# Performance work log

Hardware: AMD Instinct MI355X
Metric: run time of the kernel (lower is better)

The kernel has to match this reference:

```python
import jax, jax.numpy as jnp
import numpy as np

SEGMENTS = 64
SU2NDIM = 16
N = 16  # SU(2^4) matrix dimension
BATCH = 128


def setup_inputs() -> dict:
    key = jax.random.key(0)
    # Small scale keeps expm well-conditioned (skew-ish generators in practice)
    x = 0.1 * jax.random.normal(key, (BATCH, SEGMENTS * SU2NDIM, N, N), dtype=jnp.float32)
    return {"x": x}


def _batched_expm(a):
    # a: [..., N, N] -> expm over last two dims
    flat = a.reshape((-1, N, N))
    ex = jax.vmap(jax.scipy.linalg.expm)(flat)
    return ex.reshape(a.shape)


def reference(x):
    # maintensor = expm(-x), reversed along axis 0 (faithful to source)
    m = _batched_expm(-x)            # [B, S*D, N, N]
    m = m[::-1]                      # tf.reverse(maintensor, [0])
    b = m.shape[0]
    # tf.split along axis 1 into SEGMENTS contiguous chunks of SU2NDIM
    m = m.reshape(b, SEGMENTS, SU2NDIM, N, N)
    # Sequential chain product per segment: U = M[D-1] @ ... @ M[1] @ M[0] @ I
    ms = jnp.moveaxis(m, 2, 0)       # [D, B, S, N, N]
    u0 = jnp.broadcast_to(jnp.eye(N, dtype=x.dtype), (b, SEGMENTS, N, N))
    def step(u, mj):
        return mj @ u, None
    u, _ = jax.lax.scan(step, u0, ms)
    return u                         # [B, SEGMENTS, N, N] == transpose([1,0,2,3]) of stacked list
```

## Files before the change

### kernel.cpp

```cpp
#include <hip/hip_runtime.h>

typedef float f32x4 __attribute__((ext_vector_type(4)));
typedef short s16x8 __attribute__((ext_vector_type(8)));
typedef unsigned int uint;
typedef uint u32x4 __attribute__((ext_vector_type(4)));

union Frag {
  u32x4 u;
  s16x8 s;
};

__device__ __forceinline__ uint packhi(float f0, float f1) {
  uint a = __float_as_uint(f0) + 0x8000u;
  uint b = __float_as_uint(f1) + 0x8000u;
  return __builtin_amdgcn_perm(b, a, 0x07060302u);
}

__device__ __forceinline__ void split2(float f0, float f1, uint& hi, uint& lo) {
  uint a0 = __float_as_uint(f0) + 0x8000u;
  uint a1 = __float_as_uint(f1) + 0x8000u;
  hi = __builtin_amdgcn_perm(a1, a0, 0x07060302u);
  float h0 = __uint_as_float(a0 & 0xFFFF0000u);
  float h1 = __uint_as_float(a1 & 0xFFFF0000u);
  lo = packhi(f0 - h0, f1 - h1);
}

#define CFENCE() __asm__ __volatile__("" ::: "memory")

__device__ __forceinline__ f32x4 expm_negT(const float* __restrict__ A,
                                           uint* __restrict__ hb, int lo,
                                           int g, int gt, bool low, f32x4 idm) {
  float c0 = A[(8 * gt + 0) * 16 + lo], c1 = A[(8 * gt + 1) * 16 + lo];
  float c2 = A[(8 * gt + 2) * 16 + lo], c3 = A[(8 * gt + 3) * 16 + lo];
  float c4 = A[(8 * gt + 4) * 16 + lo], c5 = A[(8 * gt + 5) * 16 + lo];
  float c6 = A[(8 * gt + 6) * 16 + lo], c7 = A[(8 * gt + 7) * 16 + lo];
  f32x4 xr = *(const f32x4*)(A + lo * 16 + 4 * g);
  uint h, lw;
  Frag xa;
  split2(c0, c1, h, lw); xa.u[0] = low ? h : lw;
  split2(c2, c3, h, lw); xa.u[1] = low ? h : lw;
  split2(c4, c5, h, lw); xa.u[2] = low ? h : lw;
  split2(c6, c7, h, lw); xa.u[3] = low ? h : lw;
  f32x4 t;
#pragma unroll
  for (int i = 0; i < 4; ++i)
    t[i] = fmaf(1.f / 720.f, xr[i], (-1.f / 120.f) * idm[i]);
  const float SK[5] = {1.f / 24.f, -1.f / 6.f, 0.5f, -1.f, 1.f};
  uint* wp = hb + lo * 12 + 2 * g;
  const uint* rp = hb + lo * 12 + 4 * gt;
#pragma unroll
  for (int k = 0; k < 5; ++k) {
    wp[0] = packhi(t[0], t[1]);
    wp[1] = packhi(t[2], t[3]);
    CFENCE();
    Frag tb;
    tb.u = *(const u32x4*)rp;
    CFENCE();
    f32x4 acc = idm * SK[k];
    t = __builtin_amdgcn_mfma_f32_16x16x32_bf16(xa.s, tb.s, acc, 0, 0, 0);
  }
  return t;
}

__global__ __launch_bounds__(256, 8) void unitary_kernel(
    const float* __restrict__ x, float* __restrict__ out) {
  __shared__ uint HB[4][192];
  __shared__ uint PE[4][320];
  __shared__ uint PU[4][320];

  const int tid = threadIdx.x;
  const int w = tid >> 6;
  const int l = tid & 63;
  const int lo = l & 15;
  const int g = l >> 4;
  const int gt = g & 1;
  const bool low = g < 2;

  uint* hb = HB[w];
  uint* pe = PE[w];
  uint* pu = PU[w];

  const int ch = blockIdx.x * 4 + w;
  const float* xb =
      x + ((size_t)(127 - (ch >> 6)) * 1024 + (size_t)(ch & 63) * 16) * 256;

  f32x4 idm;
  idm[0] = (4 * g + 0 == lo) ? 1.f : 0.f;
  idm[1] = (4 * g + 1 == lo) ? 1.f : 0.f;
  idm[2] = (4 * g + 2 == lo) ? 1.f : 0.f;
  idm[3] = (4 * g + 3 == lo) ? 1.f : 0.f;

  Frag ifr;
  {
    uint v = ((lo >> 3) == gt) ? (0x3F80u << (16 * (lo & 1))) : 0u;
    int slot = (lo >> 1) & 3;
    ifr.u[0] = (slot == 0) ? v : 0u;
    ifr.u[1] = (slot == 1) ? v : 0u;
    ifr.u[2] = (slot == 2) ? v : 0u;
    ifr.u[3] = (slot == 3) ? v : 0u;
  }

  uint* pew = pe + lo * 20 + 4 * g;
  const uint* pea = pe + lo * 20 + 8 * gt + (low ? 0 : 2);
  uint* puw = pu + lo * 20 + 4 * g;
  const uint* pub = pu + lo * 20 + 8 * gt;

  f32x4 uc;
#pragma unroll 1
  for (int j = 0; j < 16; ++j) {
    f32x4 et = expm_negT(xb + j * 256, hb, lo, g, gt, low, idm);
    uint h0, l0, h1, l1;
    split2(et[0], et[1], h0, l0);
    split2(et[2], et[3], h1, l1);
    *(u32x4*)pew = (u32x4){h0, h1, l0, l1};
    if (j) {
      split2(uc[0], uc[1], h0, l0);
      split2(uc[2], uc[3], h1, l1);
      *(u32x4*)puw = (u32x4){h0, h1, l0, l1};
    }
    CFENCE();
    Frag ea;
    ea.u[0] = pea[0];
    ea.u[1] = pea[1];
    ea.u[2] = pea[4];
    ea.u[3] = pea[5];
    f32x4 z = {0.f, 0.f, 0.f, 0.f};
    if (j) {
      Frag b1, b2;
      b1.u[0] = pub[0];
      b1.u[1] = pub[1];
      b1.u[2] = pub[4];
      b1.u[3] = pub[5];
      b2.u[0] = pub[2];
      b2.u[1] = pub[3];
      b2.u[2] = pub[6];
      b2.u[3] = pub[7];
      CFENCE();
      f32x4 t1 = __builtin_amdgcn_mfma_f32_16x16x32_bf16(ea.s, b1.s, z, 0, 0, 0);
      uc = __builtin_amdgcn_mfma_f32_16x16x32_bf16(ea.s, b2.s, t1, 0, 0, 0);
    } else {
      CFENCE();
      uc = __builtin_amdgcn_mfma_f32_16x16x32_bf16(ea.s, ifr.s, z, 0, 0, 0);
    }
  }

  float* op = out + (size_t)ch * 256;
  op[(4 * g + 0) * 16 + lo] = uc[0];
  op[(4 * g + 1) * 16 + lo] = uc[1];
  op[(4 * g + 2) * 16 + lo] = uc[2];
  op[(4 * g + 3) * 16 + lo] = uc[3];
}

extern "C" void kernel_launch(void* const* d_in, const int* in_sizes, int n_in,
                              void* d_out, int out_size, void* d_ws,
                              size_t ws_size, hipStream_t stream) {
  const float* x = (const float*)d_in[0];
  float* out = (float*)d_out;
  unitary_kernel<<<dim3(2048), dim3(256), 0, stream>>>(x, out);
}
```

Measured before the change: 190.9 us.

## Replace LDS fragment transposes with permlane16/32 swap register shuffles

Fragment redistribution between MFMA output and input layouts was staged through per-wave shared memory (write, fence, read). It now uses v_permlane32_swap and v_permlane16_swap cross-lane exchanges held entirely in registers, for the Taylor-series operand, the exp matrix and the running product. This removes LDS traffic and its latency from the serial dependency chain, at the cost of several permlane instructions per exchange. It also frees all shared memory, which may help occupancy.

```diff
diff --git a/kernel.cpp b/kernel.cpp
--- a/kernel.cpp
+++ b/kernel.cpp
@@ -4,6 +4,7 @@
 typedef short s16x8 __attribute__((ext_vector_type(8)));
 typedef unsigned int uint;
 typedef uint u32x4 __attribute__((ext_vector_type(4)));
+typedef uint u32x2 __attribute__((ext_vector_type(2)));
 
 union Frag {
   u32x4 u;
@@ -25,10 +26,46 @@
   lo = packhi(f0 - h0, f1 - h1);
 }
 
-#define CFENCE() __asm__ __volatile__("" ::: "memory")
+__device__ __forceinline__ u32x2 swap32(uint a, uint b) {
+#if __has_builtin(__builtin_amdgcn_permlane32_swap)
+  return __builtin_amdgcn_permlane32_swap(a, b, false, false);
+#else
+  __asm__("v_permlane32_swap_b32 %0, %1" : "+v"(a), "+v"(b));
+  u32x2 r;
+  r[0] = a;
+  r[1] = b;
+  return r;
+#endif
+}
+__device__ __forceinline__ u32x2 swap16(uint a, uint b) {
+#if __has_builtin(__builtin_amdgcn_permlane16_swap)
+  return __builtin_amdgcn_permlane16_swap(a, b, false, false);
+#else
+  __asm__("v_permlane16_swap_b32 %0, %1" : "+v"(a), "+v"(b));
+  u32x2 r;
+  r[0] = a;
+  r[1] = b;
+  return r;
+#endif
+}
 
-__device__ __forceinline__ f32x4 expm_negT(const float* __restrict__ A,
-                                           uint* __restrict__ hb, int lo,
+__device__ __forceinline__ u32x4 quadB(uint p, uint q) {
+  u32x2 e = swap32(p, q);
+  u32x2 f = swap16(e[0], e[1]);
+  u32x2 r01 = swap32(f[0], f[0]);
+  u32x2 r23 = swap32(f[1], f[1]);
+  return (u32x4){r01[0], r01[1], r23[0], r23[1]};
+}
+
+__device__ __forceinline__ u32x4 quadA(uint h0, uint h1, uint l0, uint l1) {
+  u32x2 e = swap32(h0, l0);
+  u32x2 g = swap32(h1, l1);
+  u32x2 a02 = swap16(e[0], e[1]);
+  u32x2 a13 = swap16(g[0], g[1]);
+  return (u32x4){a02[0], a13[0], a02[1], a13[1]};
+}
+
+__device__ __forceinline__ f32x4 expm_negT(const float* __restrict__ A, int lo,
                                            int g, int gt, bool low, f32x4 idm) {
   float c0 = A[(8 * gt + 0) * 16 + lo], c1 = A[(8 * gt + 1) * 16 + lo];
   float c2 = A[(8 * gt + 2) * 16 + lo], c3 = A[(8 * gt + 3) * 16 + lo];
@@ -37,25 +74,23 @@
   f32x4 xr = *(const f32x4*)(A + lo * 16 + 4 * g);
   uint h, lw;
   Frag xa;
-  split2(c0, c1, h, lw); xa.u[0] = low ? h : lw;
-  split2(c2, c3, h, lw); xa.u[1] = low ? h : lw;
-  split2(c4, c5, h, lw); xa.u[2] = low ? h : lw;
-  split2(c6, c7, h, lw); xa.u[3] = low ? h : lw;
+  split2(c0, c1, h, lw);
+  xa.u[0] = low ? h : lw;
+  split2(c2, c3, h, lw);
+  xa.u[1] = low ? h : lw;
+  split2(c4, c5, h, lw);
+  xa.u[2] = low ? h : lw;
+  split2(c6, c7, h, lw);
+  xa.u[3] = low ? h : lw;
   f32x4 t;
 #pragma unroll
   for (int i = 0; i < 4; ++i)
     t[i] = fmaf(1.f / 720.f, xr[i], (-1.f / 120.f) * idm[i]);
   const float SK[5] = {1.f / 24.f, -1.f / 6.f, 0.5f, -1.f, 1.f};
-  uint* wp = hb + lo * 12 + 2 * g;
-  const uint* rp = hb + lo * 12 + 4 * gt;
 #pragma unroll
   for (int k = 0; k < 5; ++k) {
-    wp[0] = packhi(t[0], t[1]);
-    wp[1] = packhi(t[2], t[3]);
-    CFENCE();
     Frag tb;
-    tb.u = *(const u32x4*)rp;
-    CFENCE();
+    tb.u = quadB(packhi(t[0], t[1]), packhi(t[2], t[3]));
     f32x4 acc = idm * SK[k];
     t = __builtin_amdgcn_mfma_f32_16x16x32_bf16(xa.s, tb.s, acc, 0, 0, 0);
   }
@@ -64,10 +99,6 @@
 
 __global__ __launch_bounds__(256, 8) void unitary_kernel(
     const float* __restrict__ x, float* __restrict__ out) {
-  __shared__ uint HB[4][192];
-  __shared__ uint PE[4][320];
-  __shared__ uint PU[4][320];
-
   const int tid = threadIdx.x;
   const int w = tid >> 6;
   const int l = tid & 63;
@@ -75,10 +106,6 @@
   const int g = l >> 4;
   const int gt = g & 1;
   const bool low = g < 2;
-
-  uint* hb = HB[w];
-  uint* pe = PE[w];
-  uint* pu = PU[w];
 
   const int ch = blockIdx.x * 4 + w;
   const float* xb =
@@ -100,46 +127,26 @@
     ifr.u[3] = (slot == 3) ? v : 0u;
   }
 
-  uint* pew = pe + lo * 20 + 4 * g;
-  const uint* pea = pe + lo * 20 + 8 * gt + (low ? 0 : 2);
-  uint* puw = pu + lo * 20 + 4 * g;
-  const uint* pub = pu + lo * 20 + 8 * gt;
-
   f32x4 uc;
 #pragma unroll 1
   for (int j = 0; j < 16; ++j) {
-    f32x4 et = expm_negT(xb + j * 256, hb, lo, g, gt, low, idm);
-    uint h0, l0, h1, l1;
-    split2(et[0], et[1], h0, l0);
-    split2(et[2], et[3], h1, l1);
-    *(u32x4*)pew = (u32x4){h0, h1, l0, l1};
-    if (j) {
-      split2(uc[0], uc[1], h0, l0);
-      split2(uc[2], uc[3], h1, l1);
-      *(u32x4*)puw = (u32x4){h0, h1, l0, l1};
-    }
-    CFENCE();
+    f32x4 et = expm_negT(xb + j * 256, lo, g, gt, low, idm);
+    uint eh0, el0, eh1, el1;
+    split2(et[0], et[1], eh0, el0);
+    split2(et[2], et[3], eh1, el1);
     Frag ea;
-    ea.u[0] = pea[0];
-    ea.u[1] = pea[1];
-    ea.u[2] = pea[4];
-    ea.u[3] = pea[5];
+    ea.u = quadA(eh0, eh1, el0, el1);
     f32x4 z = {0.f, 0.f, 0.f, 0.f};
     if (j) {
+      uint uh0, ul0, uh1, ul1;
+      split2(uc[0], uc[1], uh0, ul0);
+      split2(uc[2], uc[3], uh1, ul1);
       Frag b1, b2;
-      b1.u[0] = pub[0];
-      b1.u[1] = pub[1];
-      b1.u[2] = pub[4];
-      b1.u[3] = pub[5];
-      b2.u[0] = pub[2];
-      b2.u[1] = pub[3];
-      b2.u[2] = pub[6];
-      b2.u[3] = pub[7];
-      CFENCE();
+      b1.u = quadB(uh0, uh1);
+      b2.u = quadB(ul0, ul1);
       f32x4 t1 = __builtin_amdgcn_mfma_f32_16x16x32_bf16(ea.s, b1.s, z, 0, 0, 0);
       uc = __builtin_amdgcn_mfma_f32_16x16x32_bf16(ea.s, b2.s, t1, 0, 0, 0);
     } else {
-      CFENCE();
       uc = __builtin_amdgcn_mfma_f32_16x16x32_bf16(ea.s, ifr.s, z, 0, 0, 0);
     }
   }
```

Measured after the change: 194.0 us. Within noise of the previous version (+1.6%).
